# Kernel optimization log

Measured on AMD Instinct MI355X. Metric: run time of the kernel, lower is better.

The kernel has to match this reference:

```python
import jax, jax.numpy as jnp
import numpy as np

# Static multi-scale spatial shapes (H, W) for a 640x640 input, strides [4,8,16,32]
SHAPES = [(160, 160), (80, 80), (40, 40), (20, 20)]
NUM_HEADS, NUM_LEVELS, NUM_POINTS, EMBED_DIM = 8, 4, 4, 256
HEAD_DIM = EMBED_DIM // NUM_HEADS
LEN_V = sum(h * w for h, w in SHAPES)  # 34000


def setup_inputs() -> dict:
    key = jax.random.key(0)
    ks = jax.random.split(key, 12)
    bs, lq = 8, 300
    inp = {
        "query": jax.random.normal(ks[0], (bs, lq, EMBED_DIM), jnp.float32),
        "reference_points": jax.random.uniform(ks[1], (bs, lq, NUM_LEVELS, 2), jnp.float32),
        "value": jax.random.normal(ks[2], (bs, LEN_V, EMBED_DIM), jnp.float32),
        "Wv": jax.random.normal(ks[3], (EMBED_DIM, EMBED_DIM), jnp.float32) * 0.02,
        "bv": jnp.zeros((EMBED_DIM,), jnp.float32),
        "Woff": jax.random.normal(ks[4], (NUM_HEADS * NUM_LEVELS * NUM_POINTS * 2, EMBED_DIM), jnp.float32) * 0.01,
        "boff": jax.random.normal(ks[5], (NUM_HEADS * NUM_LEVELS * NUM_POINTS * 2,), jnp.float32),
        "Wattn": jax.random.normal(ks[6], (NUM_HEADS * NUM_LEVELS * NUM_POINTS, EMBED_DIM), jnp.float32) * 0.02,
        "battn": jnp.zeros((NUM_HEADS * NUM_LEVELS * NUM_POINTS,), jnp.float32),
        "Wout": jax.random.normal(ks[7], (EMBED_DIM, EMBED_DIM), jnp.float32) * 0.02,
        "bout": jnp.zeros((EMBED_DIM,), jnp.float32),
    }
    return inp


def _bilinear_sample(v, loc, H, W):
    """grid_sample(align_corners=False, zero padding) equivalent.
    v:   [bs, H*W, nh, hd] level feature
    loc: [bs, Lq, nh, P, 2] sampling locations in [0, 1]
    returns [bs, Lq, nh, P, hd]
    """
    x = loc[..., 0] * W - 0.5
    y = loc[..., 1] * H - 0.5
    x0 = jnp.floor(x)
    y0 = jnp.floor(y)
    wx = (x - x0)[..., None]
    wy = (y - y0)[..., None]
    x0i = x0.astype(jnp.int32)
    y0i = y0.astype(jnp.int32)

    bs, _, nh, _ = v.shape
    bi = jnp.arange(bs)[:, None, None, None]
    hi = jnp.arange(nh)[None, None, :, None]

    def gather(xi, yi):
        valid = (xi >= 0) & (xi < W) & (yi >= 0) & (yi < H)
        idx = jnp.clip(yi, 0, H - 1) * W + jnp.clip(xi, 0, W - 1)  # [bs,Lq,nh,P]
        g = v[bi, idx, hi]  # [bs,Lq,nh,P,hd]
        return g * valid[..., None].astype(v.dtype)

    g00 = gather(x0i, y0i)
    g01 = gather(x0i + 1, y0i)
    g10 = gather(x0i, y0i + 1)
    g11 = gather(x0i + 1, y0i + 1)
    return (g00 * (1 - wx) * (1 - wy) + g01 * wx * (1 - wy)
            + g10 * (1 - wx) * wy + g11 * wx * wy)


def reference(query, reference_points, value, Wv, bv, Woff, boff, Wattn, battn, Wout, bout):
    bs, lq, _ = query.shape
    nh, nl, npts, hd = NUM_HEADS, NUM_LEVELS, NUM_POINTS, HEAD_DIM

    # value projection -> per-head value
    v = (value @ Wv.T + bv).reshape(bs, -1, nh, hd)

    # sampling offsets and attention weights from the query
    off = (query @ Woff.T + boff).reshape(bs, lq, nh, nl, npts, 2)
    aw = (query @ Wattn.T + battn).reshape(bs, lq, nh, nl * npts)
    aw = jax.nn.softmax(aw, axis=-1).reshape(bs, lq, nh, nl, npts)

    # normalize offsets by (W, H) per level; ref points are 2-d
    normalizer = jnp.array([[w, h] for h, w in SHAPES], jnp.float32)  # [nl,2]
    loc = reference_points[:, :, None, :, None, :] + off / normalizer[None, None, None, :, None, :]

    out = jnp.zeros((bs, lq, nh, hd), query.dtype)
    start = 0
    for l, (H, W) in enumerate(SHAPES):
        v_l = jax.lax.dynamic_slice_in_dim(v, start, H * W, axis=1)
        sampled = _bilinear_sample(v_l, loc[:, :, :, l], H, W)  # [bs,Lq,nh,P,hd]
        out = out + jnp.einsum("bqhp,bqhpd->bqhd", aw[:, :, :, l], sampled)
        start += H * W

    out = out.reshape(bs, lq, nh * hd)
    return out @ Wout.T + bout
```

## Files before the change

kernel.cpp:

```cpp
#include <hip/hip_runtime.h>
#include <hip/hip_bf16.h>


#define BS 8
#define LQ 300
#define LEN_V 34000
#define ED 256
#define NH 8
#define NL 4
#define NP 4

#define LDT 40

typedef short short8 __attribute__((ext_vector_type(8)));
typedef float f32x4 __attribute__((ext_vector_type(4)));

__device__ __forceinline__ void cvt8_store(__hip_bfloat16* dst, float4 a, float4 b) {
  union { short8 v; __hip_bfloat16 h[8]; } u;
  u.h[0] = __float2bfloat16(a.x); u.h[1] = __float2bfloat16(a.y);
  u.h[2] = __float2bfloat16(a.z); u.h[3] = __float2bfloat16(a.w);
  u.h[4] = __float2bfloat16(b.x); u.h[5] = __float2bfloat16(b.y);
  u.h[6] = __float2bfloat16(b.z); u.h[7] = __float2bfloat16(b.w);
  *(short8*)dst = u.v;
}

__device__ __forceinline__ void store_elem(float* p, float x) { *p = x; }
__device__ __forceinline__ void store_elem(__hip_bfloat16* p, float x) {
  *p = __float2bfloat16(x);
}

template <typename OutT>
__global__ __launch_bounds__(256) void k_gemm(
    const float* __restrict__ A, const float* __restrict__ B,
    const float* __restrict__ bias, OutT* __restrict__ C, int M, int ldc) {
  __shared__ __align__(16) __hip_bfloat16 As[128][LDT];
  __shared__ __align__(16) __hip_bfloat16 Bs[128][LDT];

  const int t = threadIdx.x;
  const size_t row0 = (size_t)blockIdx.x * 128;
  const int n0 = blockIdx.y * 128;

  const int sr = t >> 2;
  const int sc = (t & 3) * 8;

  const int wave = t >> 6;
  const int lane = t & 63;
  const int mw = (wave & 1) * 64;
  const int nw = (wave >> 1) * 64;
  const int fr = lane & 15;
  const int fk = (lane >> 4) * 8;

  f32x4 acc[4][4];
#pragma unroll
  for (int i = 0; i < 4; ++i)
#pragma unroll
    for (int j = 0; j < 4; ++j) acc[i][j] = (f32x4){0.f, 0.f, 0.f, 0.f};

  const size_t rA0 = min(row0 + sr, (size_t)(M - 1));
  const size_t rA1 = min(row0 + sr + 64, (size_t)(M - 1));
  const float* gA0 = A + rA0 * ED + sc;
  const float* gA1 = A + rA1 * ED + sc;
  const float* gB0 = B + (size_t)(n0 + sr) * ED + sc;
  const float* gB1 = B + (size_t)(n0 + sr + 64) * ED + sc;

  for (int kk = 0; kk < ED; kk += 32) {
    float4 a00 = ((const float4*)(gA0 + kk))[0];
    float4 a01 = ((const float4*)(gA0 + kk))[1];
    float4 a10 = ((const float4*)(gA1 + kk))[0];
    float4 a11 = ((const float4*)(gA1 + kk))[1];
    float4 b00 = ((const float4*)(gB0 + kk))[0];
    float4 b01 = ((const float4*)(gB0 + kk))[1];
    float4 b10 = ((const float4*)(gB1 + kk))[0];
    float4 b11 = ((const float4*)(gB1 + kk))[1];
    __syncthreads();
    cvt8_store(&As[sr][sc], a00, a01);
    cvt8_store(&As[sr + 64][sc], a10, a11);
    cvt8_store(&Bs[sr][sc], b00, b01);
    cvt8_store(&Bs[sr + 64][sc], b10, b11);
    __syncthreads();

    short8 afrag[4], bfrag[4];
#pragma unroll
    for (int mi = 0; mi < 4; ++mi)
      afrag[mi] = *(const short8*)&As[mw + mi * 16 + fr][fk];
#pragma unroll
    for (int ni = 0; ni < 4; ++ni)
      bfrag[ni] = *(const short8*)&Bs[nw + ni * 16 + fr][fk];

#pragma unroll
    for (int mi = 0; mi < 4; ++mi)
#pragma unroll
      for (int ni = 0; ni < 4; ++ni)
        acc[mi][ni] = __builtin_amdgcn_mfma_f32_16x16x32_bf16(
            afrag[mi], bfrag[ni], acc[mi][ni], 0, 0, 0);
  }

  const int rq = (lane >> 4) * 4;
#pragma unroll
  for (int ni = 0; ni < 4; ++ni) {
    const int col = n0 + nw + ni * 16 + fr;
    const float bias_v = bias[col];
#pragma unroll
    for (int mi = 0; mi < 4; ++mi) {
      const size_t rbase = row0 + mw + mi * 16 + rq;
#pragma unroll
      for (int r = 0; r < 4; ++r) {
        const size_t row = rbase + r;
        if (row < (size_t)M)
          store_elem(&C[row * (size_t)ldc + col], acc[mi][ni][r] + bias_v);
      }
    }
  }
}

__global__ __launch_bounds__(256) void k_concat(
    const float* __restrict__ Woff, const float* __restrict__ boff,
    const float* __restrict__ Wattn, const float* __restrict__ battn,
    float* __restrict__ Wcat, float* __restrict__ bcat) {
  const int row = blockIdx.x;
  const int t = threadIdx.x;
  const float* src = (row < 256) ? (Woff + (size_t)row * ED)
                                 : (Wattn + (size_t)(row - 256) * ED);
  Wcat[(size_t)row * ED + t] = src[t];
  if (t == 0) bcat[row] = (row < 256) ? boff[row] : battn[row - 256];
}

__global__ __launch_bounds__(256) void k_post(
    const float* __restrict__ refp, float* __restrict__ offs) {
  __shared__ float lg[128];
  const int t = threadIdx.x;
  const int bq = blockIdx.x;
  float* row = offs + (size_t)bq * 384;
  if (t < 128) lg[t] = row[256 + t];
  const float o = row[t];
  const int c = t & 1;
  const int l = (t >> 3) & 3;
  const float norm = (float)(160 >> l);
  const float r = refp[((size_t)bq * NL + l) * 2 + c];
  __syncthreads();
  row[t] = r + o / norm;
  if (t < NH) {
    float m = -1e30f;
#pragma unroll
    for (int i = 0; i < 16; ++i) m = fmaxf(m, lg[t * 16 + i]);
    float e[16];
    float s = 0.f;
#pragma unroll
    for (int i = 0; i < 16; ++i) {
      e[i] = expf(lg[t * 16 + i] - m);
      s += e[i];
    }
    const float inv = 1.f / s;
#pragma unroll
    for (int i = 0; i < 16; ++i) row[256 + t * 16 + i] = e[i] * inv;
  }
}

__device__ __forceinline__ float sample_one(const __hip_bfloat16* __restrict__ vb,
                                            int st, int W, int xi, int yi, int ch) {
  const bool valid = (xi >= 0) & (xi < W) & (yi >= 0) & (yi < W);
  const int xc = min(max(xi, 0), W - 1);
  const int yc = min(max(yi, 0), W - 1);
  const float g = __bfloat162float(vb[((size_t)(st + yc * W + xc)) * ED + ch]);
  return valid ? g : 0.f;
}

__global__ __launch_bounds__(512) void k_sample(
    const __hip_bfloat16* __restrict__ v, const float* __restrict__ offs,
    float* __restrict__ inner) {
  __shared__ float part[16][256];
  __shared__ float slo[256];
  __shared__ float saw[128];
  const int t = threadIdx.x;
  const int bq = blockIdx.x;
  const int b = bq / LQ;
  const float* rowq = offs + (size_t)bq * 384;
  if (t < 256) slo[t] = rowq[t];
  else if (t < 384) saw[t - 256] = rowq[t];
  __syncthreads();

  const int pi = t >> 5;
  const int d = t & 31;
  const int l = pi >> 2;
  const int p = pi & 3;
  const int W = 160 >> l;
  const int st = (l == 0) ? 0 : (l == 1) ? 25600 : (l == 2) ? 32000 : 33600;
  const __hip_bfloat16* vb = v + (size_t)b * LEN_V * ED;

#pragma unroll
  for (int h = 0; h < NH; ++h) {
    const int base = ((h * NL + l) * NP + p) * 2;
    const float lx = slo[base];
    const float ly = slo[base + 1];
    const float w = saw[h * 16 + pi];
    const float x = lx * (float)W - 0.5f;
    const float y = ly * (float)W - 0.5f;
    const float x0f = floorf(x);
    const float y0f = floorf(y);
    const float wx = x - x0f;
    const float wy = y - y0f;
    const int x0 = (int)x0f;
    const int y0 = (int)y0f;
    const int ch = h * 32 + d;
    const float g00 = sample_one(vb, st, W, x0, y0, ch);
    const float g01 = sample_one(vb, st, W, x0 + 1, y0, ch);
    const float g10 = sample_one(vb, st, W, x0, y0 + 1, ch);
    const float g11 = sample_one(vb, st, W, x0 + 1, y0 + 1, ch);
    const float vxy = (g00 * (1.f - wx) + g01 * wx) * (1.f - wy) +
                      (g10 * (1.f - wx) + g11 * wx) * wy;
    part[pi][ch] = w * vxy;
  }
  __syncthreads();
  if (t < 256) {
    float s = 0.f;
#pragma unroll
    for (int q = 0; q < 16; ++q) s += part[q][t];
    inner[(size_t)bq * ED + t] = s;
  }
}

extern "C" void kernel_launch(void* const* d_in, const int* in_sizes, int n_in,
                              void* d_out, int out_size, void* d_ws, size_t ws_size,
                              hipStream_t stream) {
  const float* query = (const float*)d_in[0];
  const float* refp  = (const float*)d_in[1];
  const float* value = (const float*)d_in[2];
  const float* Wv    = (const float*)d_in[3];
  const float* bv    = (const float*)d_in[4];
  const float* Woff  = (const float*)d_in[5];
  const float* boff  = (const float*)d_in[6];
  const float* Wattn = (const float*)d_in[7];
  const float* battn = (const float*)d_in[8];
  const float* Wout  = (const float*)d_in[9];
  const float* bout  = (const float*)d_in[10];
  float* out = (float*)d_out;

  char* ws = (char*)d_ws;
  __hip_bfloat16* v = (__hip_bfloat16*)ws;
  size_t off = (size_t)BS * LEN_V * ED * 2;
  float* offs = (float*)(ws + off);
  off += (size_t)BS * LQ * 384 * 4;
  float* inner = (float*)(ws + off);
  off += (size_t)BS * LQ * 256 * 4;
  float* Wcat = (float*)(ws + off);
  off += (size_t)384 * ED * 4;
  float* bcat = (float*)(ws + off);

  const int M_Q = BS * LQ;

  k_concat<<<384, 256, 0, stream>>>(Woff, boff, Wattn, battn, Wcat, bcat);
  k_gemm<__hip_bfloat16><<<dim3(2125, 2), 256, 0, stream>>>(
      value, Wv, bv, v, BS * LEN_V, ED);
  k_gemm<float><<<dim3(19, 3), 256, 0, stream>>>(
      query, Wcat, bcat, offs, M_Q, 384);
  k_post<<<M_Q, 256, 0, stream>>>(refp, offs);
  k_sample<<<M_Q, 512, 0, stream>>>(v, offs, inner);
  k_gemm<float><<<dim3(19, 2), 256, 0, stream>>>(
      inner, Wout, bout, out, M_Q, ED);
}
```

Measured before the change: 599.2 us.

## Use persistent value-projection kernel with whole weight resident in LDS

Replaces the tiled value-projection GEMM with a persistent kernel of 256 blocks. Each block converts the full 256x256 weight to bf16 once in shared memory, then loops over 128-row strips of the value tensor. A-fragments are loaded straight from global into registers with one-step prefetch, and output tiles are staged through shared memory for coalesced 16-byte stores. This removes the repeated A/B shared-memory staging and the duplicate reads of A across two N-blocks. In exchange it uses a large LDS footprint per block, which limits occupancy, and adds extra barriers in the store phase.

New measurement: 554.5 us. -7.5%, faster.

```diff
diff --git a/kernel.cpp b/kernel.cpp
--- a/kernel.cpp
+++ b/kernel.cpp
@@ -12,21 +12,133 @@
 
 #define LDT 40
 
+#define VSTRIPS 2125
+
 typedef short short8 __attribute__((ext_vector_type(8)));
+typedef short sv4 __attribute__((ext_vector_type(4)));
 typedef float f32x4 __attribute__((ext_vector_type(4)));
 
-__device__ __forceinline__ void cvt8_store(__hip_bfloat16* dst, float4 a, float4 b) {
+__device__ __forceinline__ short8 cvt8_reg(float4 a, float4 b) {
   union { short8 v; __hip_bfloat16 h[8]; } u;
   u.h[0] = __float2bfloat16(a.x); u.h[1] = __float2bfloat16(a.y);
   u.h[2] = __float2bfloat16(a.z); u.h[3] = __float2bfloat16(a.w);
   u.h[4] = __float2bfloat16(b.x); u.h[5] = __float2bfloat16(b.y);
   u.h[6] = __float2bfloat16(b.z); u.h[7] = __float2bfloat16(b.w);
-  *(short8*)dst = u.v;
+  return u.v;
+}
+
+__device__ __forceinline__ void cvt8_store(__hip_bfloat16* dst, float4 a, float4 b) {
+  *(short8*)dst = cvt8_reg(a, b);
 }
 
 __device__ __forceinline__ void store_elem(float* p, float x) { *p = x; }
 __device__ __forceinline__ void store_elem(__hip_bfloat16* p, float x) {
   *p = __float2bfloat16(x);
+}
+
+__global__ __launch_bounds__(512) void k_vproj(
+    const float* __restrict__ A, const float* __restrict__ B,
+    const float* __restrict__ bias, __hip_bfloat16* __restrict__ C) {
+  __shared__ __align__(16) __hip_bfloat16 Bs[256][264];
+  __shared__ __align__(16) __hip_bfloat16 Cs[32][264];
+
+  const int t = threadIdx.x;
+
+  for (int i = t; i < 256 * 64; i += 512) {
+    const int n = i >> 6;
+    const int kf = (i & 63) * 4;
+    const float4 b4 = *(const float4*)(B + (size_t)n * ED + kf);
+    union { sv4 v; __hip_bfloat16 h[4]; } u;
+    u.h[0] = __float2bfloat16(b4.x);
+    u.h[1] = __float2bfloat16(b4.y);
+    u.h[2] = __float2bfloat16(b4.z);
+    u.h[3] = __float2bfloat16(b4.w);
+    *(sv4*)&Bs[n][kf] = u.v;
+  }
+  __syncthreads();
+
+  const int wave = t >> 6;
+  const int lane = t & 63;
+  const int wr = wave >> 2;
+  const int wc = wave & 3;
+  const int fr = lane & 15;
+  const int fk = (lane >> 4) * 8;
+  const int rq = (lane >> 4) * 4;
+
+  float bias_v[4];
+#pragma unroll
+  for (int ni = 0; ni < 4; ++ni) bias_v[ni] = bias[wc * 64 + ni * 16 + fr];
+
+  for (int strip = blockIdx.x; strip < VSTRIPS; strip += gridDim.x) {
+    const size_t row0 = (size_t)strip * 128;
+    const float* gA = A + (row0 + wr * 64 + fr) * ED + fk;
+
+    f32x4 acc[4][4];
+#pragma unroll
+    for (int i = 0; i < 4; ++i)
+#pragma unroll
+      for (int j = 0; j < 4; ++j) acc[i][j] = (f32x4){0.f, 0.f, 0.f, 0.f};
+
+    float4 c0[4], c1[4];
+#pragma unroll
+    for (int mi = 0; mi < 4; ++mi) {
+      c0[mi] = *(const float4*)(gA + mi * 16 * ED);
+      c1[mi] = *(const float4*)(gA + mi * 16 * ED + 4);
+    }
+
+    for (int kk = 0; kk < ED; kk += 32) {
+      float4 p0[4], p1[4];
+      if (kk < ED - 32) {
+#pragma unroll
+        for (int mi = 0; mi < 4; ++mi) {
+          p0[mi] = *(const float4*)(gA + mi * 16 * ED + kk + 32);
+          p1[mi] = *(const float4*)(gA + mi * 16 * ED + kk + 36);
+        }
+      }
+      short8 af[4], bf[4];
+#pragma unroll
+      for (int mi = 0; mi < 4; ++mi) af[mi] = cvt8_reg(c0[mi], c1[mi]);
+#pragma unroll
+      for (int ni = 0; ni < 4; ++ni)
+        bf[ni] = *(const short8*)&Bs[wc * 64 + ni * 16 + fr][kk + fk];
+#pragma unroll
+      for (int mi = 0; mi < 4; ++mi)
+#pragma unroll
+        for (int ni = 0; ni < 4; ++ni)
+          acc[mi][ni] = __builtin_amdgcn_mfma_f32_16x16x32_bf16(
+              af[mi], bf[ni], acc[mi][ni], 0, 0, 0);
+#pragma unroll
+      for (int mi = 0; mi < 4; ++mi) { c0[mi] = p0[mi]; c1[mi] = p1[mi]; }
+    }
+
+#pragma unroll
+    for (int p = 0; p < 4; ++p) {
+      if (wr == (p >> 1)) {
+        const int mib = (p & 1) * 2;
+#pragma unroll
+        for (int ni = 0; ni < 4; ++ni) {
+          const int col = wc * 64 + ni * 16 + fr;
+#pragma unroll
+          for (int mj = 0; mj < 2; ++mj) {
+            const int mi = mib + mj;
+            const int rl = mj * 16 + rq;
+#pragma unroll
+            for (int r = 0; r < 4; ++r)
+              Cs[rl + r][col] = __float2bfloat16(acc[mi][ni][r] + bias_v[ni]);
+          }
+        }
+      }
+      __syncthreads();
+      {
+        const int rr = t >> 5;
+        const int cb = (t & 31) * 8;
+        const size_t gr = row0 + p * 32;
+        *(short8*)(C + (gr + rr) * ED + cb) = *(const short8*)&Cs[rr][cb];
+        *(short8*)(C + (gr + rr + 16) * ED + cb) = *(const short8*)&Cs[rr + 16][cb];
+      }
+      __syncthreads();
+    }
+  }
 }
 
 template <typename OutT>
@@ -249,8 +361,7 @@
   const int M_Q = BS * LQ;
 
   k_concat<<<384, 256, 0, stream>>>(Woff, boff, Wattn, battn, Wcat, bcat);
-  k_gemm<__hip_bfloat16><<<dim3(2125, 2), 256, 0, stream>>>(
-      value, Wv, bv, v, BS * LEN_V, ED);
+  k_vproj<<<256, 512, 0, stream>>>(value, Wv, bv, v);
   k_gemm<float><<<dim3(19, 3), 256, 0, stream>>>(
       query, Wcat, bcat, offs, M_Q, 384);
   k_post<<<M_Q, 256, 0, stream>>>(refp, offs);
```
